# Performance work log

Measured on AMD Instinct MI355X. Metric: run time of the kernel, lower is better.

The kernel has to match this reference:

```python
import jax, jax.numpy as jnp
import numpy as np
import math

NUM_HEADS = 16


def setup_inputs() -> dict:
    key = jax.random.key(0)
    ks = jax.random.split(key, 5)
    L, B, E = 2048, 2, 1024
    scale = 1.0 / math.sqrt(E)
    return {
        "query": jax.random.normal(ks[0], (L, B, E), jnp.float32),
        "key": jax.random.normal(ks[1], (L, B, E), jnp.float32),
        "value": jax.random.normal(ks[2], (L, B, E), jnp.float32),
        "in_proj_weight": jax.random.normal(ks[3], (3 * E, E), jnp.float32) * scale,
        "in_proj_bias": jnp.zeros((3 * E,), jnp.float32),
        "out_w": jax.random.normal(ks[4], (E, E), jnp.float32) * scale,
        "out_b": jnp.zeros((E,), jnp.float32),
    }


def reference(query, key, value, in_proj_weight, in_proj_bias, out_w, out_b):
    L, Bz, E = query.shape
    S = key.shape[0]
    H = NUM_HEADS
    hd = E // H
    # in-projection: chunk packed weight into q/k/v parts (same math as torch chunk)
    w_q, w_k, w_v = jnp.split(in_proj_weight, 3, axis=0)
    b_q, b_k, b_v = jnp.split(in_proj_bias, 3, axis=0)
    q = query @ w_q.T + b_q            # (L, B, E)
    k = key @ w_k.T + b_k              # (S, B, E)
    v = value @ w_v.T + b_v            # (S, B, E)
    # (L, B*H, hd) -> (B*H, L, hd)
    q = q.reshape(L, Bz * H, hd).transpose(1, 0, 2) / math.sqrt(hd)
    k = k.reshape(S, Bz * H, hd).transpose(1, 0, 2)
    v = v.reshape(S, Bz * H, hd).transpose(1, 0, 2)
    # sigmoid attention (non-softmax), full (B*H, L, S) matrix as in original
    attn = jax.nn.sigmoid(jnp.einsum("bld,bsd->bls", q, k))
    denom = attn.sum(axis=-1, keepdims=True) + 1e-4
    out = jnp.einsum("bls,bsd->bld", attn / denom, v)  # (B*H, L, hd)
    out = out.transpose(1, 0, 2).reshape(L, Bz, E)
    out = out @ out_w.T + out_b
    avg_weights = attn.reshape(Bz, H, L, S).sum(axis=1) / H
    return out, avg_weights
```

## Files before the change

kernel.cpp:

```cpp
#include <hip/hip_runtime.h>
#include <stdint.h>


#define L_SEQ 2048
#define NBATCH 2
#define EMB 1024
#define NHEAD 16
#define HD 64
#define MROWS 4096

typedef __bf16 bf16x8 __attribute__((ext_vector_type(8)));
typedef float f32x4 __attribute__((ext_vector_type(4)));

__device__ __forceinline__ unsigned short f2bf(float f) {
  union { float f; uint32_t u; } v; v.f = f;
  uint32_t u = v.u;
  u += 0x7fffu + ((u >> 16) & 1u);
  return (unsigned short)(u >> 16);
}

__device__ __forceinline__ void gl_lds16(const void* gptr, void* ldsptr) {
  const uint32_t* g = reinterpret_cast<const uint32_t*>(gptr);
  auto* l = reinterpret_cast<__attribute__((address_space(3))) uint32_t*>(
      reinterpret_cast<uintptr_t>(ldsptr));
  __builtin_amdgcn_global_load_lds(g, l, 16, 0, 0);
}

__device__ __forceinline__ f32x4 mfma16(bf16x8 a, bf16x8 b, f32x4 c) {
  return __builtin_amdgcn_mfma_f32_16x16x32_bf16(a, b, c, 0, 0, 0);
}

__device__ __forceinline__ float fast_sigmoid(float x) {
  float e = __expf(-x);
  return __builtin_amdgcn_rcpf(1.0f + e);
}

__global__ __launch_bounds__(256) void k_convert(
    const float* __restrict__ qin, const float* __restrict__ kin,
    const float* __restrict__ vin, const float* __restrict__ win,
    const float* __restrict__ wo,
    unsigned short* __restrict__ Xq, unsigned short* __restrict__ Xk,
    unsigned short* __restrict__ Xv, unsigned short* __restrict__ Wb,
    unsigned short* __restrict__ Wob) {
  const int row = blockIdx.x;
  const int t = threadIdx.x;
  const float* src;
  unsigned short* dst;
  int srow;
  size_t drow;
  if (row < 3 * MROWS) {
    const int which = row >> 12;
    const int m = row & (MROWS - 1);
    const int b = m >> 11, l = m & (L_SEQ - 1);
    srow = l * NBATCH + b;
    drow = (size_t)m;
    src = which == 0 ? qin : (which == 1 ? kin : vin);
    dst = which == 0 ? Xq : (which == 1 ? Xk : Xv);
  } else if (row < 3 * MROWS + 3072) {
    srow = row - 3 * MROWS; drow = (size_t)srow; src = win; dst = Wb;
  } else {
    srow = row - (3 * MROWS + 3072); drow = (size_t)srow; src = wo; dst = Wob;
  }
  const float4 vv = *(const float4*)(src + (size_t)srow * EMB + t * 4);
  ushort4 o;
  o.x = f2bf(vv.x); o.y = f2bf(vv.y); o.z = f2bf(vv.z); o.w = f2bf(vv.w);
  *(ushort4*)(dst + drow * EMB + t * 4) = o;
}

__device__ __forceinline__ void gemm_core(
    const unsigned short* __restrict__ A, const unsigned short* __restrict__ Bm,
    int m0, int n0, unsigned short* sA, unsigned short* sB, f32x4 acc[4][4]) {
  const int tid = threadIdx.x;
  const int wave = tid >> 6;
  const int lane = tid & 63;
  const int quad = lane >> 4;
  const int l16 = lane & 15;
  const int wm = (wave >> 1) * 64;
  const int wn = (wave & 1) * 64;
  const int srow = lane >> 2;
  const int scol = lane & 3;

  for (int mi = 0; mi < 4; ++mi)
    for (int ni = 0; ni < 4; ++ni)
      acc[mi][ni] = (f32x4){0.f, 0.f, 0.f, 0.f};

  for (int k0 = 0; k0 < EMB; k0 += 32) {
    __syncthreads();
    for (int i = 0; i < 2; ++i) {
      const int p = wave * 2 + i;
      const int r = p * 16 + srow;
      const int c = scol ^ ((r >> 1) & 3);
      gl_lds16(A + (size_t)(m0 + r) * EMB + k0 + c * 8, sA + p * 512);
      gl_lds16(Bm + (size_t)(n0 + r) * EMB + k0 + c * 8, sB + p * 512);
    }
    __syncthreads();
    bf16x8 af[4], bfr[4];
    for (int mi = 0; mi < 4; ++mi) {
      const int r = wm + mi * 16 + l16;
      const int cp = quad ^ ((r >> 1) & 3);
      af[mi] = *(const bf16x8*)(sA + r * 32 + cp * 8);
    }
    for (int ni = 0; ni < 4; ++ni) {
      const int r = wn + ni * 16 + l16;
      const int cp = quad ^ ((r >> 1) & 3);
      bfr[ni] = *(const bf16x8*)(sB + r * 32 + cp * 8);
    }
    for (int mi = 0; mi < 4; ++mi)
      for (int ni = 0; ni < 4; ++ni)
        acc[mi][ni] = mfma16(af[mi], bfr[ni], acc[mi][ni]);
  }
}

__global__ __launch_bounds__(256) void k_inproj(
    const unsigned short* __restrict__ Xq, const unsigned short* __restrict__ Xk,
    const unsigned short* __restrict__ Xv, const unsigned short* __restrict__ Wb,
    const float* __restrict__ bias,
    unsigned short* __restrict__ qb, unsigned short* __restrict__ kb,
    unsigned short* __restrict__ vb) {
  __shared__ __attribute__((aligned(16))) unsigned short sA[128 * 32];
  __shared__ __attribute__((aligned(16))) unsigned short sB[128 * 32];
  const int z = blockIdx.z;
  const unsigned short* A = z == 0 ? Xq : (z == 1 ? Xk : Xv);
  const int n0 = blockIdx.x * 128, m0 = blockIdx.y * 128;
  f32x4 acc[4][4];
  gemm_core(A, Wb + (size_t)z * EMB * EMB, m0, n0, sA, sB, acc);

  const int tid = threadIdx.x, wave = tid >> 6, lane = tid & 63;
  const int quad = lane >> 4, l16 = lane & 15;
  const int wm = (wave >> 1) * 64, wn = (wave & 1) * 64;
  const float scale = (z == 0) ? 0.125f : 1.0f;
  unsigned short* dst01 = (z == 0) ? qb : kb;
  for (int ni = 0; ni < 4; ++ni) {
    const int n = n0 + wn + ni * 16 + l16;
    const float bv = bias[z * EMB + n];
    const int h = n >> 6, d = n & 63;
    for (int mi = 0; mi < 4; ++mi) {
      for (int r = 0; r < 4; ++r) {
        const int m = m0 + wm + mi * 16 + quad * 4 + r;
        const int b = m >> 11, l = m & (L_SEQ - 1);
        const unsigned short o = f2bf((acc[mi][ni][r] + bv) * scale);
        if (z == 2)
          vb[((size_t)(b * NHEAD + h) * HD + d) * L_SEQ + l] = o;
        else
          dst01[((size_t)(b * NHEAD + h) * L_SEQ + l) * HD + d] = o;
      }
    }
  }
}

__global__ __launch_bounds__(256) void k_attn(
    const unsigned short* __restrict__ qb, const unsigned short* __restrict__ kb,
    const unsigned short* __restrict__ vb, unsigned short* __restrict__ oh) {
  __shared__ __attribute__((aligned(16))) unsigned short sQ[128 * 64];
  __shared__ __attribute__((aligned(16))) unsigned short sK[64 * 64];
  __shared__ __attribute__((aligned(16))) unsigned short sV[64 * 64];
  __shared__ __attribute__((aligned(16))) unsigned short sP[128 * 72];
  __shared__ float sDen[128];

  const int bh = blockIdx.x;
  const int b = bh >> 4, h = bh & 15;
  const int l0 = blockIdx.y * 128;
  const unsigned short* qg = qb + ((size_t)bh * L_SEQ + l0) * HD;
  const unsigned short* kg = kb + (size_t)bh * L_SEQ * HD;
  const unsigned short* vg = vb + (size_t)bh * HD * L_SEQ;

  const int tid = threadIdx.x, wave = tid >> 6, lane = tid & 63;
  const int quad = lane >> 4, l16 = lane & 15;
  const int lw = wave * 32;
  const int sr8 = lane >> 3;
  const int sc8 = lane & 7;

  for (int i = 0; i < 4; ++i) {
    const int p = wave * 4 + i;
    const int r = p * 8 + sr8;
    const int c = sc8 ^ (r & 7);
    gl_lds16(qg + (size_t)r * HD + c * 8, sQ + p * 512);
  }

  f32x4 oacc[2][4];
  for (int mi = 0; mi < 2; ++mi)
    for (int ni = 0; ni < 4; ++ni) oacc[mi][ni] = (f32x4){0.f, 0.f, 0.f, 0.f};
  float den[2] = {0.f, 0.f};

  for (int s0 = 0; s0 < L_SEQ; s0 += 64) {
    __syncthreads();
    for (int i = 0; i < 2; ++i) {
      const int p = wave * 2 + i;
      const int r = p * 8 + sr8;
      const int c = sc8 ^ (r & 7);
      gl_lds16(kg + (size_t)(s0 + r) * HD + c * 8, sK + p * 512);
      gl_lds16(vg + (size_t)r * L_SEQ + s0 + c * 8, sV + p * 512);
    }
    __syncthreads();

    f32x4 st[4][2];
    for (int smi = 0; smi < 4; ++smi)
      for (int lni = 0; lni < 2; ++lni) st[smi][lni] = (f32x4){0.f, 0.f, 0.f, 0.f};
    for (int kk = 0; kk < HD; kk += 32) {
      bf16x8 a[4], bq[2];
      for (int smi = 0; smi < 4; ++smi) {
        const int r = smi * 16 + l16;
        const int c = ((kk >> 3) + quad) ^ (r & 7);
        a[smi] = *(const bf16x8*)(sK + r * 64 + c * 8);
      }
      for (int lni = 0; lni < 2; ++lni) {
        const int r = lw + lni * 16 + l16;
        const int c = ((kk >> 3) + quad) ^ (r & 7);
        bq[lni] = *(const bf16x8*)(sQ + r * 64 + c * 8);
      }
      for (int smi = 0; smi < 4; ++smi)
        for (int lni = 0; lni < 2; ++lni)
          st[smi][lni] = mfma16(a[smi], bq[lni], st[smi][lni]);
    }

    for (int lni = 0; lni < 2; ++lni) {
      const int lrow = lw + lni * 16 + l16;
      for (int smi = 0; smi < 4; ++smi) {
        const float p0 = fast_sigmoid(st[smi][lni][0]);
        const float p1 = fast_sigmoid(st[smi][lni][1]);
        const float p2 = fast_sigmoid(st[smi][lni][2]);
        const float p3 = fast_sigmoid(st[smi][lni][3]);
        den[lni] += (p0 + p1) + (p2 + p3);
        ushort4 pk;
        pk.x = f2bf(p0); pk.y = f2bf(p1); pk.z = f2bf(p2); pk.w = f2bf(p3);
        *(ushort4*)(sP + (size_t)lrow * 72 + smi * 16 + quad * 4) = pk;
      }
    }
    __syncthreads();

    for (int kk = 0; kk < 64; kk += 32) {
      bf16x8 ap[2], bv4[4];
      for (int mi = 0; mi < 2; ++mi) {
        const int r = lw + mi * 16 + l16;
        ap[mi] = *(const bf16x8*)(sP + r * 72 + kk + quad * 8);
      }
      for (int ni = 0; ni < 4; ++ni) {
        const int rd = ni * 16 + l16;
        const int c = ((kk >> 3) + quad) ^ (rd & 7);
        bv4[ni] = *(const bf16x8*)(sV + rd * 64 + c * 8);
      }
      for (int mi = 0; mi < 2; ++mi)
        for (int ni = 0; ni < 4; ++ni)
          oacc[mi][ni] = mfma16(ap[mi], bv4[ni], oacc[mi][ni]);
    }
  }

  for (int lni = 0; lni < 2; ++lni) {
    float d2 = den[lni];
    d2 += __shfl_xor(d2, 16, 64);
    d2 += __shfl_xor(d2, 32, 64);
    if (quad == 0) sDen[lw + lni * 16 + l16] = __builtin_amdgcn_rcpf(d2 + 1e-4f);
  }
  __syncthreads();

  for (int mi = 0; mi < 2; ++mi) {
    for (int r = 0; r < 4; ++r) {
      const int lrow = lw + mi * 16 + quad * 4 + r;
      const float rden = sDen[lrow];
      unsigned short* dst =
          oh + ((size_t)(b * L_SEQ + l0 + lrow)) * EMB + h * HD;
      for (int ni = 0; ni < 4; ++ni)
        dst[ni * 16 + l16] = f2bf(oacc[mi][ni][r] * rden);
    }
  }
}

__global__ __launch_bounds__(256) void k_avg(
    const unsigned short* __restrict__ qb, const unsigned short* __restrict__ kb,
    float* __restrict__ avg) {
  __shared__ __attribute__((aligned(16))) unsigned short sQ[128 * 64];
  __shared__ __attribute__((aligned(16))) unsigned short sK[128 * 64];
  const int ss0 = blockIdx.x * 128, l0 = blockIdx.y * 128, b = blockIdx.z;
  const int tid = threadIdx.x, wave = tid >> 6, lane = tid & 63;
  const int quad = lane >> 4, l16 = lane & 15;
  const int wm = (wave >> 1) * 64, wn = (wave & 1) * 64;
  const int sr8 = lane >> 3, sc8 = lane & 7;

  f32x4 av[4][4];
  for (int mi = 0; mi < 4; ++mi)
    for (int ni = 0; ni < 4; ++ni) av[mi][ni] = (f32x4){0.f, 0.f, 0.f, 0.f};

  for (int h = 0; h < NHEAD; ++h) {
    const unsigned short* qg = qb + ((size_t)(b * NHEAD + h) * L_SEQ + l0) * HD;
    const unsigned short* kg = kb + ((size_t)(b * NHEAD + h) * L_SEQ + ss0) * HD;
    __syncthreads();
    for (int i = 0; i < 4; ++i) {
      const int p = wave * 4 + i;
      const int r = p * 8 + sr8;
      const int c = sc8 ^ (r & 7);
      gl_lds16(qg + (size_t)r * HD + c * 8, sQ + p * 512);
      gl_lds16(kg + (size_t)r * HD + c * 8, sK + p * 512);
    }
    __syncthreads();
    f32x4 scr[4][4];
    for (int mi = 0; mi < 4; ++mi)
      for (int ni = 0; ni < 4; ++ni) scr[mi][ni] = (f32x4){0.f, 0.f, 0.f, 0.f};
    for (int kk = 0; kk < HD; kk += 32) {
      bf16x8 a[4], bb[4];
      for (int mi = 0; mi < 4; ++mi) {
        const int r = wm + mi * 16 + l16;
        const int c = ((kk >> 3) + quad) ^ (r & 7);
        a[mi] = *(const bf16x8*)(sQ + r * 64 + c * 8);
      }
      for (int ni = 0; ni < 4; ++ni) {
        const int r = wn + ni * 16 + l16;
        const int c = ((kk >> 3) + quad) ^ (r & 7);
        bb[ni] = *(const bf16x8*)(sK + r * 64 + c * 8);
      }
      for (int mi = 0; mi < 4; ++mi)
        for (int ni = 0; ni < 4; ++ni)
          scr[mi][ni] = mfma16(a[mi], bb[ni], scr[mi][ni]);
    }
    for (int mi = 0; mi < 4; ++mi)
      for (int ni = 0; ni < 4; ++ni)
        for (int r = 0; r < 4; ++r)
          av[mi][ni][r] += fast_sigmoid(scr[mi][ni][r]);
  }

  for (int mi = 0; mi < 4; ++mi) {
    for (int r = 0; r < 4; ++r) {
      const int l = l0 + wm + mi * 16 + quad * 4 + r;
      float* dst = avg + ((size_t)b * L_SEQ + l) * L_SEQ + ss0 + wn;
      for (int ni = 0; ni < 4; ++ni)
        dst[ni * 16 + l16] = av[mi][ni][r] * 0.0625f;
    }
  }
}

__global__ __launch_bounds__(256) void k_outproj(
    const unsigned short* __restrict__ OH, const unsigned short* __restrict__ Wob,
    const float* __restrict__ ob, float* __restrict__ out) {
  __shared__ __attribute__((aligned(16))) unsigned short sA[128 * 32];
  __shared__ __attribute__((aligned(16))) unsigned short sB[128 * 32];
  const int n0 = blockIdx.x * 128, m0 = blockIdx.y * 128;
  f32x4 acc[4][4];
  gemm_core(OH, Wob, m0, n0, sA, sB, acc);

  const int tid = threadIdx.x, wave = tid >> 6, lane = tid & 63;
  const int quad = lane >> 4, l16 = lane & 15;
  const int wm = (wave >> 1) * 64, wn = (wave & 1) * 64;
  for (int ni = 0; ni < 4; ++ni) {
    const int n = n0 + wn + ni * 16 + l16;
    const float bv = ob[n];
    for (int mi = 0; mi < 4; ++mi) {
      for (int r = 0; r < 4; ++r) {
        const int m = m0 + wm + mi * 16 + quad * 4 + r;
        const int b = m >> 11, l = m & (L_SEQ - 1);
        out[((size_t)l * NBATCH + b) * EMB + n] = acc[mi][ni][r] + bv;
      }
    }
  }
}

extern "C" void kernel_launch(void* const* d_in, const int* in_sizes, int n_in,
                              void* d_out, int out_size, void* d_ws, size_t ws_size,
                              hipStream_t stream) {
  (void)in_sizes; (void)n_in; (void)out_size;
  const float* qin = (const float*)d_in[0];
  const float* kin = (const float*)d_in[1];
  const float* vin = (const float*)d_in[2];
  const float* w   = (const float*)d_in[3];
  const float* bias = (const float*)d_in[4];
  const float* wo  = (const float*)d_in[5];
  const float* ob  = (const float*)d_in[6];
  float* out = (float*)d_out;

  unsigned short* Xq  = (unsigned short*)d_ws;
  unsigned short* Xk  = Xq + (size_t)MROWS * EMB;
  unsigned short* Xv  = Xk + (size_t)MROWS * EMB;
  unsigned short* Wb  = Xv + (size_t)MROWS * EMB;
  unsigned short* Wob = Wb + (size_t)3 * EMB * EMB;
  unsigned short* qbuf = Wob + (size_t)EMB * EMB;
  unsigned short* kbuf = qbuf + (size_t)MROWS * EMB;
  unsigned short* vbuf = kbuf + (size_t)MROWS * EMB;
  unsigned short* ohb  = vbuf + (size_t)MROWS * EMB;
  const size_t need = ((size_t)MROWS * EMB * 7 + (size_t)4 * EMB * EMB) * 2;
  if (ws_size < need) return;

  k_convert<<<16384, 256, 0, stream>>>(qin, kin, vin, w, wo, Xq, Xk, Xv, Wb, Wob);
  k_inproj<<<dim3(8, 32, 3), 256, 0, stream>>>(Xq, Xk, Xv, Wb, bias, qbuf, kbuf, vbuf);
  k_attn<<<dim3(32, 16), 256, 0, stream>>>(qbuf, kbuf, vbuf, ohb);
  k_avg<<<dim3(16, 16, 2), 256, 0, stream>>>(qbuf, kbuf, out + (size_t)MROWS * EMB);
  k_outproj<<<dim3(8, 32), 256, 0, stream>>>(ohb, Wob, ob, out);
}
```

Before: 304.0 us.

## Use 512-thread blocks for attention and averaging kernels, denominator via MFMA

```diff
diff --git a/kernel.cpp b/kernel.cpp
--- a/kernel.cpp
+++ b/kernel.cpp
@@ -17,6 +17,11 @@
   uint32_t u = v.u;
   u += 0x7fffu + ((u >> 16) & 1u);
   return (unsigned short)(u >> 16);
+}
+
+__device__ __forceinline__ unsigned short f2bf_fast(float f) {
+  union { float f; uint32_t u; } v; v.f = f;
+  return (unsigned short)((v.u + 0x8000u) >> 16);
 }
 
 __device__ __forceinline__ void gl_lds16(const void* gptr, void* ldsptr) {
@@ -148,14 +153,13 @@
   }
 }
 
-__global__ __launch_bounds__(256) void k_attn(
+__global__ __launch_bounds__(512) void k_attn(
     const unsigned short* __restrict__ qb, const unsigned short* __restrict__ kb,
     const unsigned short* __restrict__ vb, unsigned short* __restrict__ oh) {
   __shared__ __attribute__((aligned(16))) unsigned short sQ[128 * 64];
   __shared__ __attribute__((aligned(16))) unsigned short sK[64 * 64];
   __shared__ __attribute__((aligned(16))) unsigned short sV[64 * 64];
   __shared__ __attribute__((aligned(16))) unsigned short sP[128 * 72];
-  __shared__ float sDen[128];
 
   const int bh = blockIdx.x;
   const int b = bh >> 4, h = bh & 15;
@@ -166,106 +170,103 @@
 
   const int tid = threadIdx.x, wave = tid >> 6, lane = tid & 63;
   const int quad = lane >> 4, l16 = lane & 15;
-  const int lw = wave * 32;
-  const int sr8 = lane >> 3;
-  const int sc8 = lane & 7;
-
-  for (int i = 0; i < 4; ++i) {
-    const int p = wave * 4 + i;
+  const int sr8 = lane >> 3, sc8 = lane & 7;
+  const int sh = (wave >> 2) * 32;
+  const int lq = (wave & 3) * 32;
+
+  for (int i = 0; i < 2; ++i) {
+    const int p = wave * 2 + i;
     const int r = p * 8 + sr8;
     const int c = sc8 ^ (r & 7);
     gl_lds16(qg + (size_t)r * HD + c * 8, sQ + p * 512);
   }
 
-  f32x4 oacc[2][4];
-  for (int mi = 0; mi < 2; ++mi)
-    for (int ni = 0; ni < 4; ++ni) oacc[mi][ni] = (f32x4){0.f, 0.f, 0.f, 0.f};
-  float den[2] = {0.f, 0.f};
+  f32x4 oacc[4];
+  for (int ni = 0; ni < 4; ++ni) oacc[ni] = (f32x4){0.f, 0.f, 0.f, 0.f};
+  f32x4 dacc = (f32x4){0.f, 0.f, 0.f, 0.f};
+
+  bf16x8 ones;
+  for (int j = 0; j < 8; ++j) ones[j] = (__bf16)1.0f;
 
   for (int s0 = 0; s0 < L_SEQ; s0 += 64) {
     __syncthreads();
-    for (int i = 0; i < 2; ++i) {
-      const int p = wave * 2 + i;
-      const int r = p * 8 + sr8;
-      const int c = sc8 ^ (r & 7);
-      gl_lds16(kg + (size_t)(s0 + r) * HD + c * 8, sK + p * 512);
-      gl_lds16(vg + (size_t)r * L_SEQ + s0 + c * 8, sV + p * 512);
-    }
-    __syncthreads();
-
-    f32x4 st[4][2];
-    for (int smi = 0; smi < 4; ++smi)
+    if (wave < 4) {
+      for (int i = 0; i < 2; ++i) {
+        const int p = wave * 2 + i;
+        const int r = p * 8 + sr8;
+        const int c = sc8 ^ (r & 7);
+        gl_lds16(kg + (size_t)(s0 + r) * HD + c * 8, sK + p * 512);
+      }
+    } else {
+      for (int i = 0; i < 2; ++i) {
+        const int p = (wave - 4) * 2 + i;
+        const int r = p * 8 + sr8;
+        const int c = sc8 ^ (r & 7);
+        gl_lds16(vg + (size_t)r * L_SEQ + s0 + c * 8, sV + p * 512);
+      }
+    }
+    __syncthreads();
+
+    f32x4 st[2][2];
+    for (int smi = 0; smi < 2; ++smi)
       for (int lni = 0; lni < 2; ++lni) st[smi][lni] = (f32x4){0.f, 0.f, 0.f, 0.f};
     for (int kk = 0; kk < HD; kk += 32) {
-      bf16x8 a[4], bq[2];
-      for (int smi = 0; smi < 4; ++smi) {
-        const int r = smi * 16 + l16;
+      bf16x8 a[2], bq[2];
+      for (int smi = 0; smi < 2; ++smi) {
+        const int r = sh + smi * 16 + l16;
         const int c = ((kk >> 3) + quad) ^ (r & 7);
         a[smi] = *(const bf16x8*)(sK + r * 64 + c * 8);
       }
       for (int lni = 0; lni < 2; ++lni) {
-        const int r = lw + lni * 16 + l16;
+        const int r = lq + lni * 16 + l16;
         const int c = ((kk >> 3) + quad) ^ (r & 7);
         bq[lni] = *(const bf16x8*)(sQ + r * 64 + c * 8);
       }
-      for (int smi = 0; smi < 4; ++smi)
+      for (int smi = 0; smi < 2; ++smi)
         for (int lni = 0; lni < 2; ++lni)
           st[smi][lni] = mfma16(a[smi], bq[lni], st[smi][lni]);
     }
 
     for (int lni = 0; lni < 2; ++lni) {
-      const int lrow = lw + lni * 16 + l16;
-      for (int smi = 0; smi < 4; ++smi) {
-        const float p0 = fast_sigmoid(st[smi][lni][0]);
-        const float p1 = fast_sigmoid(st[smi][lni][1]);
-        const float p2 = fast_sigmoid(st[smi][lni][2]);
-        const float p3 = fast_sigmoid(st[smi][lni][3]);
-        den[lni] += (p0 + p1) + (p2 + p3);
-        ushort4 pk;
-        pk.x = f2bf(p0); pk.y = f2bf(p1); pk.z = f2bf(p2); pk.w = f2bf(p3);
-        *(ushort4*)(sP + (size_t)lrow * 72 + smi * 16 + quad * 4) = pk;
-      }
-    }
-    __syncthreads();
-
+      const int lrow = lq + lni * 16 + l16;
+      for (int smi = 0; smi < 2; ++smi) {
+        uint32_t u[4];
+        for (int r = 0; r < 4; ++r) {
+          union { float f; uint32_t i; } cv;
+          cv.f = fast_sigmoid(st[smi][lni][r]);
+          u[r] = cv.i + 0x8000u;
+        }
+        uint2 pk;
+        pk.x = __builtin_amdgcn_perm(u[1], u[0], 0x07060302u);
+        pk.y = __builtin_amdgcn_perm(u[3], u[2], 0x07060302u);
+        *(uint2*)(sP + (size_t)lrow * 72 + sh + smi * 16 + quad * 4) = pk;
+      }
+    }
+    __syncthreads();
+
+    const int lr = wave * 16 + l16;
     for (int kk = 0; kk < 64; kk += 32) {
-      bf16x8 ap[2], bv4[4];
-      for (int mi = 0; mi < 2; ++mi) {
-        const int r = lw + mi * 16 + l16;
-        ap[mi] = *(const bf16x8*)(sP + r * 72 + kk + quad * 8);
-      }
+      bf16x8 ap = *(const bf16x8*)(sP + (size_t)lr * 72 + kk + quad * 8);
       for (int ni = 0; ni < 4; ++ni) {
         const int rd = ni * 16 + l16;
         const int c = ((kk >> 3) + quad) ^ (rd & 7);
-        bv4[ni] = *(const bf16x8*)(sV + rd * 64 + c * 8);
-      }
-      for (int mi = 0; mi < 2; ++mi)
-        for (int ni = 0; ni < 4; ++ni)
-          oacc[mi][ni] = mfma16(ap[mi], bv4[ni], oacc[mi][ni]);
-    }
-  }
-
-  for (int lni = 0; lni < 2; ++lni) {
-    float d2 = den[lni];
-    d2 += __shfl_xor(d2, 16, 64);
-    d2 += __shfl_xor(d2, 32, 64);
-    if (quad == 0) sDen[lw + lni * 16 + l16] = __builtin_amdgcn_rcpf(d2 + 1e-4f);
-  }
-  __syncthreads();
-
-  for (int mi = 0; mi < 2; ++mi) {
-    for (int r = 0; r < 4; ++r) {
-      const int lrow = lw + mi * 16 + quad * 4 + r;
-      const float rden = sDen[lrow];
-      unsigned short* dst =
-          oh + ((size_t)(b * L_SEQ + l0 + lrow)) * EMB + h * HD;
-      for (int ni = 0; ni < 4; ++ni)
-        dst[ni * 16 + l16] = f2bf(oacc[mi][ni][r] * rden);
-    }
-  }
-}
-
-__global__ __launch_bounds__(256) void k_avg(
+        bf16x8 bv4 = *(const bf16x8*)(sV + rd * 64 + c * 8);
+        oacc[ni] = mfma16(ap, bv4, oacc[ni]);
+      }
+      dacc = mfma16(ap, ones, dacc);
+    }
+  }
+
+  for (int r = 0; r < 4; ++r) {
+    const int lrow = l0 + wave * 16 + quad * 4 + r;
+    const float rden = __builtin_amdgcn_rcpf(dacc[r] + 1e-4f);
+    unsigned short* dst = oh + ((size_t)(b * L_SEQ + lrow)) * EMB + h * HD;
+    for (int ni = 0; ni < 4; ++ni)
+      dst[ni * 16 + l16] = f2bf_fast(oacc[ni][r] * rden);
+  }
+}
+
+__global__ __launch_bounds__(512) void k_avg(
     const unsigned short* __restrict__ qb, const unsigned short* __restrict__ kb,
     float* __restrict__ avg) {
   __shared__ __attribute__((aligned(16))) unsigned short sQ[128 * 64];
@@ -273,46 +274,46 @@
   const int ss0 = blockIdx.x * 128, l0 = blockIdx.y * 128, b = blockIdx.z;
   const int tid = threadIdx.x, wave = tid >> 6, lane = tid & 63;
   const int quad = lane >> 4, l16 = lane & 15;
-  const int wm = (wave >> 1) * 64, wn = (wave & 1) * 64;
+  const int wm = (wave & 1) * 64, wn = (wave >> 1) * 32;
   const int sr8 = lane >> 3, sc8 = lane & 7;
 
-  f32x4 av[4][4];
+  f32x4 av[4][2];
   for (int mi = 0; mi < 4; ++mi)
-    for (int ni = 0; ni < 4; ++ni) av[mi][ni] = (f32x4){0.f, 0.f, 0.f, 0.f};
+    for (int ni = 0; ni < 2; ++ni) av[mi][ni] = (f32x4){0.f, 0.f, 0.f, 0.f};
 
   for (int h = 0; h < NHEAD; ++h) {
     const unsigned short* qg = qb + ((size_t)(b * NHEAD + h) * L_SEQ + l0) * HD;
     const unsigned short* kg = kb + ((size_t)(b * NHEAD + h) * L_SEQ + ss0) * HD;
     __syncthreads();
-    for (int i = 0; i < 4; ++i) {
-      const int p = wave * 4 + i;
+    for (int i = 0; i < 2; ++i) {
+      const int p = wave * 2 + i;
       const int r = p * 8 + sr8;
       const int c = sc8 ^ (r & 7);
       gl_lds16(qg + (size_t)r * HD + c * 8, sQ + p * 512);
       gl_lds16(kg + (size_t)r * HD + c * 8, sK + p * 512);
     }
     __syncthreads();
-    f32x4 scr[4][4];
+    f32x4 scr[4][2];
     for (int mi = 0; mi < 4; ++mi)
-      for (int ni = 0; ni < 4; ++ni) scr[mi][ni] = (f32x4){0.f, 0.f, 0.f, 0.f};
+      for (int ni = 0; ni < 2; ++ni) scr[mi][ni] = (f32x4){0.f, 0.f, 0.f, 0.f};
     for (int kk = 0; kk < HD; kk += 32) {
-      bf16x8 a[4], bb[4];
+      bf16x8 a[4], bb[2];
       for (int mi = 0; mi < 4; ++mi) {
         const int r = wm + mi * 16 + l16;
         const int c = ((kk >> 3) + quad) ^ (r & 7);
         a[mi] = *(const bf16x8*)(sQ + r * 64 + c * 8);
       }
-      for (int ni = 0; ni < 4; ++ni) {
+      for (int ni = 0; ni < 2; ++ni) {
         const int r = wn + ni * 16 + l16;
         const int c = ((kk >> 3) + quad) ^ (r & 7);
         bb[ni] = *(const bf16x8*)(sK + r * 64 + c * 8);
       }
       for (int mi = 0; mi < 4; ++mi)
-        for (int ni = 0; ni < 4; ++ni)
+        for (int ni = 0; ni < 2; ++ni)
           scr[mi][ni] = mfma16(a[mi], bb[ni], scr[mi][ni]);
     }
     for (int mi = 0; mi < 4; ++mi)
-      for (int ni = 0; ni < 4; ++ni)
+      for (int ni = 0; ni < 2; ++ni)
         for (int r = 0; r < 4; ++r)
           av[mi][ni][r] += fast_sigmoid(scr[mi][ni][r]);
   }
@@ -321,7 +322,7 @@
     for (int r = 0; r < 4; ++r) {
       const int l = l0 + wm + mi * 16 + quad * 4 + r;
       float* dst = avg + ((size_t)b * L_SEQ + l) * L_SEQ + ss0 + wn;
-      for (int ni = 0; ni < 4; ++ni)
+      for (int ni = 0; ni < 2; ++ni)
         dst[ni * 16 + l16] = av[mi][ni][r] * 0.0625f;
     }
   }
@@ -379,7 +380,7 @@
 
   k_convert<<<16384, 256, 0, stream>>>(qin, kin, vin, w, wo, Xq, Xk, Xv, Wb, Wob);
   k_inproj<<<dim3(8, 32, 3), 256, 0, stream>>>(Xq, Xk, Xv, Wb, bias, qbuf, kbuf, vbuf);
-  k_attn<<<dim3(32, 16), 256, 0, stream>>>(qbuf, kbuf, vbuf, ohb);
-  k_avg<<<dim3(16, 16, 2), 256, 0, stream>>>(qbuf, kbuf, out + (size_t)MROWS * EMB);
+  k_attn<<<dim3(32, 16), 512, 0, stream>>>(qbuf, kbuf, vbuf, ohb);
+  k_avg<<<dim3(16, 16, 2), 512, 0, stream>>>(qbuf, kbuf, out + (size_t)MROWS * EMB);
   k_outproj<<<dim3(8, 32), 256, 0, stream>>>(ohb, Wob, ob, out);
 }
```

After: 275.7 us. 9.3% less time.
